# Performance work log

Hardware: AMD Instinct MI355X
Metric: run time of the kernel (lower is better)

The kernel has to match this reference:

```python
import jax, jax.numpy as jnp
import numpy as np

BS, L, H, D = 4, 1024, 12, 768   # docs, seq len, attn heads, hidden
NE, M, P = 42, 96, 42 * 42        # max entities (min_height), mentions/doc, ht pairs
OFFSET = 1                        # bert/roberta [CLS] offset


def setup_inputs() -> dict:
    key = jax.random.key(0)
    k1, k2, k3, k4, k5 = jax.random.split(key, 5)
    sequence_output = jax.random.normal(k1, (BS, L, D), jnp.float32)
    attention = jax.random.uniform(k2, (BS, H, L, L), jnp.float32)
    mention_pos = jax.random.randint(k3, (BS, M), 0, L - OFFSET - 1).astype(jnp.int32)
    mention_entity = jnp.sort(jax.random.randint(k4, (BS, M), 0, NE), axis=-1).astype(jnp.int32)
    hts = jax.random.randint(k5, (BS, P, 2), 0, NE).astype(jnp.int32)
    return {"sequence_output": sequence_output, "attention": attention,
            "mention_pos": mention_pos, "mention_entity": mention_entity, "hts": hts}


def _per_doc_entities(seq, att, pos, ent):
    # seq [L,D], att [H,L,L], pos [M] mention token idx, ent [M] entity segment id
    idx = pos + OFFSET
    m_emb = seq[idx]                              # [M,D]  gathered mention embeddings
    m_att = jnp.transpose(att[:, idx], (1, 0, 2))  # [M,H,L] gathered mention attentions
    counts = jax.ops.segment_sum(jnp.ones((M,), seq.dtype), ent, num_segments=NE)
    has = counts > 0
    # mean-pool attentions per entity (zeros for empty entities, as in torch code)
    e_att = jax.ops.segment_sum(m_att, ent, num_segments=NE) / jnp.maximum(counts, 1.0)[:, None, None]
    # stable logsumexp-pool embeddings per entity
    seg_max = jax.ops.segment_max(m_emb, ent, num_segments=NE)      # -inf for empty segments
    seg_max = jnp.where(has[:, None], seg_max, 0.0)
    seg_sum = jax.ops.segment_sum(jnp.exp(m_emb - seg_max[ent]), ent, num_segments=NE)
    e_emb = jnp.where(has[:, None], jnp.log(jnp.maximum(seg_sum, 1e-30)) + seg_max, 0.0)
    return e_emb, e_att                           # [NE,D], [NE,H,L]


def _channel_map(seq, e_att):
    # all-pairs (h_att * t_att).mean(heads), normalize over tokens, contract with seq
    pair = jnp.einsum('ahl,bhl->abl', e_att, e_att) / H      # [NE,NE,L]
    pair = pair / (pair.sum(-1, keepdims=True) + 1e-5)
    return jnp.einsum('abl,ld->abd', pair, seq)              # [NE,NE,D]


def reference(sequence_output, attention, mention_pos, mention_entity, hts):
    e_emb, e_att = jax.vmap(_per_doc_entities)(sequence_output, attention,
                                               mention_pos, mention_entity)
    hss = jax.vmap(lambda emb, ht: emb[ht[:, 0]])(e_emb, hts).reshape(BS * P, D)
    tss = jax.vmap(lambda emb, ht: emb[ht[:, 1]])(e_emb, hts).reshape(BS * P, D)
    feature_map = jax.vmap(_channel_map)(sequence_output, e_att)  # [BS,NE,NE,D]
    return hss, tss, feature_map
```

## Files before the change

### kernel.cpp

```cpp
#include <hip/hip_runtime.h>
#include <hip/hip_bf16.h>

#define BSZ   4
#define LSEQ  1024
#define NH    12
#define DDIM  768
#define NEN   42
#define NM    96
#define NPAIR (NEN*NEN)
#define OFF   1

typedef short bf16x8 __attribute__((ext_vector_type(8)));
typedef float f32x4  __attribute__((ext_vector_type(4)));

__device__ __forceinline__ float bf2f(unsigned short u) {
    union { unsigned u; float f; } c; c.u = ((unsigned)u) << 16; return c.f;
}

typedef const __attribute__((address_space(1))) unsigned int glb_u32;
typedef __attribute__((address_space(3))) unsigned int lds_u32;
__device__ __forceinline__ void glds16(const void* g, void* l) {
    __builtin_amdgcn_global_load_lds((glb_u32*)g, (lds_u32*)l, 16, 0, 0);
}

#define EMB_CNT  (BSZ*NEN*DDIM)
#define EATT_CNT (BSZ*NEN*NH*LSEQ)
#define PTIL_CNT ((size_t)BSZ*NPAIR*LSEQ)

#define PREP_EMB_BLKS  (BSZ*NEN*3)
#define PREP_ATT_BLKS  (BSZ*NEN*NH)
#define PREP_T_BLKS    ((LSEQ/32)*(DDIM/32)*BSZ)
#define PREP_TOTAL     (PREP_EMB_BLKS + PREP_ATT_BLKS + PREP_T_BLKS)

#define TEN   6
#define NTILE 7
#define NTRIT (NTILE*(NTILE+1)/2)
#define LCHK  256
#define PAIR_TOTAL (NTRIT*(LSEQ/LCHK)*BSZ)

#define BM 128
#define BN 64
#define BK 64
#define MT 14
#define NT (DDIM/BN)
#define FMAP_BLKS (MT*NT*BSZ)
#define GATH_BLKS (BSZ*NPAIR/4)
#define TAIL_TOTAL (FMAP_BLKS + GATH_BLKS)

__global__ __launch_bounds__(256) void prep_kernel(
        const float* __restrict__ seq,
        const float* __restrict__ att,
        const int* __restrict__ mpos,
        const int* __restrict__ ment,
        float* __restrict__ e_emb,
        __hip_bfloat16* __restrict__ e_att,
        __hip_bfloat16* __restrict__ seqT) {
    __shared__ __align__(16) char smraw[4352];
    const int bid = blockIdx.x;
    const int t = threadIdx.x;

    if (bid < PREP_EMB_BLKS) {
        int chunk = bid % 3;
        int e = (bid / 3) % NEN;
        int b = bid / (3 * NEN);
        int* sp   = (int*)smraw;
        int* se   = sp + NM;
        int* list = se + NM;
        int* pcnt = list + NM;
        if (t < NM) { sp[t] = mpos[b*NM + t] + OFF; se[t] = ment[b*NM + t]; }
        __syncthreads();
        if (t == 0) {
            int c = 0;
            for (int m = 0; m < NM; ++m) if (se[m] == e) list[c++] = sp[m];
            pcnt[0] = c;
        }
        __syncthreads();
        int cnt = pcnt[0];
        int d = chunk * 256 + t;
        const float* sq = seq + (size_t)b * LSEQ * DDIM + d;
        float mx = -1e30f;
        for (int m = 0; m < cnt; ++m) mx = fmaxf(mx, sq[(size_t)list[m] * DDIM]);
        float out = 0.f;
        if (cnt) {
            float s = 0.f;
            for (int m = 0; m < cnt; ++m) s += expf(sq[(size_t)list[m] * DDIM] - mx);
            out = logf(fmaxf(s, 1e-30f)) + mx;
        }
        e_emb[((size_t)b*NEN + e)*DDIM + d] = out;
    } else if (bid < PREP_EMB_BLKS + PREP_ATT_BLKS) {
        int id = bid - PREP_EMB_BLKS;
        int h = id % NH;
        int e = (id / NH) % NEN;
        int b = id / (NH * NEN);
        int* sp = (int*)smraw;
        int* se = sp + NM;
        if (t < NM) { sp[t] = mpos[b*NM + t] + OFF; se[t] = ment[b*NM + t]; }
        __syncthreads();
        const float* ab = att + ((size_t)(b*NH + h)) * LSEQ * LSEQ;
        float4 acc = {0.f, 0.f, 0.f, 0.f};
        int cnt = 0;
        for (int m = 0; m < NM; ++m) {
            if (se[m] == e) {
                ++cnt;
                float4 v = ((const float4*)(ab + (size_t)sp[m]*LSEQ))[t];
                acc.x += v.x; acc.y += v.y; acc.z += v.z; acc.w += v.w;
            }
        }
        float inv = cnt ? 1.f / (float)cnt : 0.f;
        union { ushort4 u4; __hip_bfloat16 hh[4]; } pk;
        pk.hh[0] = __float2bfloat16(acc.x * inv);
        pk.hh[1] = __float2bfloat16(acc.y * inv);
        pk.hh[2] = __float2bfloat16(acc.z * inv);
        pk.hh[3] = __float2bfloat16(acc.w * inv);
        ((ushort4*)(e_att + ((size_t)(b*NEN + e)*NH + h)*LSEQ))[t] = pk.u4;
    } else {
        int id = bid - PREP_EMB_BLKS - PREP_ATT_BLKS;
        int l0 = (id % (LSEQ/32)) * 32;
        int d0 = ((id / (LSEQ/32)) % (DDIM/32)) * 32;
        int b  = id / ((LSEQ/32) * (DDIM/32));
        float (*tile)[33] = (float(*)[33])smraw;
        int l = t >> 3, dq = (t & 7) * 4;
        float4 v = *(const float4*)(seq + ((size_t)b*LSEQ + l0 + l)*DDIM + d0 + dq);
        tile[l][dq+0] = v.x; tile[l][dq+1] = v.y;
        tile[l][dq+2] = v.z; tile[l][dq+3] = v.w;
        __syncthreads();
        int d = t >> 3, lq = (t & 7) * 4;
        union { ushort4 u4; __hip_bfloat16 h[4]; } pk;
        pk.h[0] = __float2bfloat16(tile[lq+0][d]);
        pk.h[1] = __float2bfloat16(tile[lq+1][d]);
        pk.h[2] = __float2bfloat16(tile[lq+2][d]);
        pk.h[3] = __float2bfloat16(tile[lq+3][d]);
        *(ushort4*)(seqT + ((size_t)b*DDIM + d0 + d)*LSEQ + l0 + lq) = pk.u4;
    }
}

__global__ __launch_bounds__(256) void pair_tile_kernel(
        const __hip_bfloat16* __restrict__ e_att,
        __hip_bfloat16* __restrict__ ptil) {
    const int bid = blockIdx.x;
    const int t = threadIdx.x;
    int tri = bid % NTRIT;
    int lc  = (bid / NTRIT) % (LSEQ/LCHK);
    int b   = bid / (NTRIT * (LSEQ/LCHK));
    int ta = 0, rem = tri;
    while (rem >= NTILE - ta) { rem -= NTILE - ta; ++ta; }
    int tb = ta + rem;
    int l = lc * LCHK + t;

    const __hip_bfloat16* ebase = e_att + (size_t)b*NEN*NH*LSEQ + l;
    float s[TEN][TEN];
    #pragma unroll
    for (int i = 0; i < TEN; ++i)
        #pragma unroll
        for (int j = 0; j < TEN; ++j) s[i][j] = 0.f;

    #pragma unroll 4
    for (int h = 0; h < NH; ++h) {
        float xa[TEN], xb[TEN];
        #pragma unroll
        for (int e = 0; e < TEN; ++e)
            xa[e] = bf2f(*(const unsigned short*)(ebase + ((size_t)(ta*TEN+e)*NH + h)*LSEQ));
        #pragma unroll
        for (int e = 0; e < TEN; ++e)
            xb[e] = bf2f(*(const unsigned short*)(ebase + ((size_t)(tb*TEN+e)*NH + h)*LSEQ));
        #pragma unroll
        for (int i = 0; i < TEN; ++i)
            #pragma unroll
            for (int j = 0; j < TEN; ++j)
                s[i][j] += xa[i] * xb[j];
    }

    __hip_bfloat16* pbase = ptil + (size_t)b*NPAIR*LSEQ + l;
    #pragma unroll
    for (int i = 0; i < TEN; ++i) {
        #pragma unroll
        for (int j = 0; j < TEN; ++j) {
            union { unsigned short u; __hip_bfloat16 h; } pk;
            pk.h = __float2bfloat16(s[i][j]);
            int pa = ta*TEN + i, pb = tb*TEN + j;
            *(unsigned short*)(pbase + (size_t)(pa*NEN + pb)*LSEQ) = pk.u;
            if (ta != tb)
                *(unsigned short*)(pbase + (size_t)(pb*NEN + pa)*LSEQ) = pk.u;
        }
    }
}

__global__ __launch_bounds__(256) void tail_kernel(
        const __hip_bfloat16* __restrict__ ptil,
        const __hip_bfloat16* __restrict__ seqT,
        const float* __restrict__ e_emb,
        const int* __restrict__ hts,
        float* __restrict__ out_h,
        float* __restrict__ out_t,
        float* __restrict__ fmap) {
    __shared__ __hip_bfloat16 As[2][BM*BK];
    __shared__ __hip_bfloat16 Bs[2][BN*BK];
    const int bid = blockIdx.x;
    const int t = threadIdx.x;

    if (bid >= FMAP_BLKS) {
        int id4  = bid - FMAP_BLKS;
        int grp  = t >> 6;
        int lane = t & 63;
        int id   = id4 * 4 + grp;
        int b    = id / NPAIR;
        int hi = hts[id*2 + 0];
        int ti = hts[id*2 + 1];
        const float4* eh = (const float4*)(e_emb + ((size_t)(b*NEN + hi))*DDIM);
        const float4* et = (const float4*)(e_emb + ((size_t)(b*NEN + ti))*DDIM);
        float4* oh = (float4*)(out_h + (size_t)id*DDIM);
        float4* ot = (float4*)(out_t + (size_t)id*DDIM);
        #pragma unroll
        for (int i = 0; i < 3; ++i) {
            oh[lane + 64*i] = eh[lane + 64*i];
            ot[lane + 64*i] = et[lane + 64*i];
        }
        return;
    }

    const int lane = t & 63;
    const int wid  = t >> 6;
    const int wr   = wid >> 1;
    const int wc   = wid & 1;
    const int bx = bid % MT, by = (bid / MT) % NT, b = bid / (MT*NT);
    const int r0 = bx * BM, c0 = by * BN;

    const char* Ab  = (const char*)(ptil + (size_t)b * NPAIR * LSEQ);
    const char* Btb = (const char*)(seqT + (size_t)b * DDIM * LSEQ);
    char* AsB = (char*)As;
    char* BsB = (char*)Bs;

    const f32x4 zero = {0.f, 0.f, 0.f, 0.f};
    f32x4 acc[4][2];
    #pragma unroll
    for (int m = 0; m < 4; ++m)
        #pragma unroll
        for (int n = 0; n < 2; ++n) acc[m][n] = zero;

    const int fr = lane & 15, kg = lane >> 4;
    const int rs_r = t >> 1, rs_h = t & 1;
    float rsum = 0.f;

#define STAGE(buf, k0)                                                        \
    {                                                                         \
        _Pragma("unroll")                                                     \
        for (int i = 0; i < 4; ++i) {                                         \
            int L = wid*4096 + i*1024 + lane*16;                              \
            int r = L >> 7, beta = L & 127;                                   \
            glds16(Ab + (size_t)(r0 + r)*(LSEQ*2) + (k0)*2                    \
                      + (beta ^ ((r & 7) << 4)), AsB + (buf)*16384 + L);      \
        }                                                                     \
        _Pragma("unroll")                                                     \
        for (int i = 0; i < 2; ++i) {                                         \
            int L = wid*2048 + i*1024 + lane*16;                              \
            int c = L >> 7, beta = L & 127;                                   \
            glds16(Btb + (size_t)(c0 + c)*(LSEQ*2) + (k0)*2                   \
                      + (beta ^ ((c & 7) << 4)), BsB + (buf)*8192 + L);       \
        }                                                                     \
    }

    STAGE(0, 0);
    __syncthreads();

    int cur = 0;
    for (int ki = 0; ki < LSEQ/BK; ++ki) {
        if (ki + 1 < LSEQ/BK) STAGE(cur ^ 1, (ki + 1) * BK);

        const __hip_bfloat16* Ac = (const __hip_bfloat16*)(AsB + cur*16384);
        const __hip_bfloat16* Bc = (const __hip_bfloat16*)(BsB + cur*8192);

        #pragma unroll
        for (int jj = 0; jj < 4; ++jj) {
            int e0 = (rs_h*32 + jj*8) ^ ((rs_r & 7) << 3);
            bf16x8 v = *(const bf16x8*)(Ac + rs_r*64 + e0);
            #pragma unroll
            for (int j = 0; j < 8; ++j) rsum += bf2f((unsigned short)v[j]);
        }

        #pragma unroll
        for (int ks = 0; ks < 2; ++ks) {
            bf16x8 af[4], bfv[2];
            #pragma unroll
            for (int m = 0; m < 4; ++m) {
                int R = wr*64 + m*16 + fr;
                int e0 = (ks*32 + kg*8) ^ ((R & 7) << 3);
                af[m] = *(const bf16x8*)(Ac + R*64 + e0);
            }
            #pragma unroll
            for (int n = 0; n < 2; ++n) {
                int C = wc*32 + n*16 + fr;
                int e0 = (ks*32 + kg*8) ^ ((C & 7) << 3);
                bfv[n] = *(const bf16x8*)(Bc + C*64 + e0);
            }
            #pragma unroll
            for (int m = 0; m < 4; ++m)
                #pragma unroll
                for (int n = 0; n < 2; ++n)
                    acc[m][n] = __builtin_amdgcn_mfma_f32_16x16x32_bf16(
                                    af[m], bfv[n], acc[m][n], 0, 0, 0);
        }
        __syncthreads();
        cur ^= 1;
    }

    float rtot = rsum + __shfl_down(rsum, 1);
    float* ssum = (float*)AsB;
    if ((t & 1) == 0) ssum[rs_r] = rtot;
    __syncthreads();

    #pragma unroll
    for (int m = 0; m < 4; ++m) {
        int lr0 = wr*64 + m*16 + kg*4;
        #pragma unroll
        for (int i = 0; i < 4; ++i) {
            int lr = lr0 + i;
            int row = r0 + lr;
            if (row < NPAIR) {
                float sc = 1.f / (ssum[lr] + (float)NH * 1e-5f);
                #pragma unroll
                for (int n = 0; n < 2; ++n) {
                    int col = c0 + wc*32 + n*16 + fr;
                    fmap[((size_t)b*NPAIR + row)*DDIM + col] = acc[m][n][i] * sc;
                }
            }
        }
    }
#undef STAGE
}

extern "C" void kernel_launch(void* const* d_in, const int* in_sizes, int n_in,
                              void* d_out, int out_size, void* d_ws, size_t ws_size,
                              hipStream_t stream) {
    const float* seq  = (const float*)d_in[0];
    const float* att  = (const float*)d_in[1];
    const int*   mpos = (const int*)d_in[2];
    const int*   ment = (const int*)d_in[3];
    const int*   hts  = (const int*)d_in[4];

    float* ws_f  = (float*)d_ws;
    float* e_emb = ws_f;
    __hip_bfloat16* e_att = (__hip_bfloat16*)(ws_f + EMB_CNT);
    __hip_bfloat16* ptil  = e_att + EATT_CNT;
    __hip_bfloat16* seqT  = ptil + PTIL_CNT;

    float* out_h = (float*)d_out;
    float* out_t = out_h + (size_t)BSZ*NPAIR*DDIM;
    float* fmap  = out_t + (size_t)BSZ*NPAIR*DDIM;

    hipLaunchKernelGGL(prep_kernel, dim3(PREP_TOTAL), dim3(256), 0, stream,
                       seq, att, mpos, ment, e_emb, e_att, seqT);
    hipLaunchKernelGGL(pair_tile_kernel, dim3(PAIR_TOTAL), dim3(256), 0, stream,
                       e_att, ptil);
    hipLaunchKernelGGL(tail_kernel, dim3(TAIL_TOTAL), dim3(256), 0, stream,
                       ptil, seqT, e_emb, hts, out_h, out_t, fmap);
}
```

Before: 59.73 us.

## Rebalance kernel stages and compute pair row sums in pair-tile kernel

Splits the entity attention pooling into its own kernel and moves the seq transpose and embedding pooling into the pair-tile kernel, so independent work overlaps with pair-product computation. The pair-tile blocks now reduce per-row sums over their L chunk in fp32 and write partial sums to a workspace. The GEMM tail reads those partials instead of summing the A tile from LDS each K step. Tail block indices are also remapped across groups of eight. This removes per-iteration ALU and LDS work from the GEMM loop. It adds a shuffle reduction and extra small global writes in the pair stage.

Result: faster. 56.17 us (-6.0%).

```diff
diff --git a/kernel.cpp b/kernel.cpp
--- a/kernel.cpp
+++ b/kernel.cpp
@@ -23,20 +23,22 @@
     __builtin_amdgcn_global_load_lds((glb_u32*)g, (lds_u32*)l, 16, 0, 0);
 }
 
+#define NLC   4
 #define EMB_CNT  (BSZ*NEN*DDIM)
+#define PSUM_CNT (BSZ*NLC*NPAIR)
 #define EATT_CNT (BSZ*NEN*NH*LSEQ)
 #define PTIL_CNT ((size_t)BSZ*NPAIR*LSEQ)
 
-#define PREP_EMB_BLKS  (BSZ*NEN*3)
-#define PREP_ATT_BLKS  (BSZ*NEN*NH)
-#define PREP_T_BLKS    ((LSEQ/32)*(DDIM/32)*BSZ)
-#define PREP_TOTAL     (PREP_EMB_BLKS + PREP_ATT_BLKS + PREP_T_BLKS)
+#define ATT_TOTAL (BSZ*NEN*NH)
 
 #define TEN   6
 #define NTILE 7
 #define NTRIT (NTILE*(NTILE+1)/2)
 #define LCHK  256
-#define PAIR_TOTAL (NTRIT*(LSEQ/LCHK)*BSZ)
+#define PAIR_BLKS (NTRIT*NLC*BSZ)
+#define T_BLKS    ((LSEQ/32)*(DDIM/32)*BSZ)
+#define EMB_BLKS  (BSZ*NEN*3)
+#define MID2_TOTAL (PAIR_BLKS + T_BLKS + EMB_BLKS)
 
 #define BM 128
 #define BN 64
@@ -47,22 +49,148 @@
 #define GATH_BLKS (BSZ*NPAIR/4)
 #define TAIL_TOTAL (FMAP_BLKS + GATH_BLKS)
 
-__global__ __launch_bounds__(256) void prep_kernel(
-        const float* __restrict__ seq,
+__global__ __launch_bounds__(256) void att_kernel(
         const float* __restrict__ att,
         const int* __restrict__ mpos,
         const int* __restrict__ ment,
-        float* __restrict__ e_emb,
-        __hip_bfloat16* __restrict__ e_att,
-        __hip_bfloat16* __restrict__ seqT) {
+        __hip_bfloat16* __restrict__ e_att) {
+    __shared__ int sp[NM];
+    __shared__ int se[NM];
+    int id = blockIdx.x;
+    int h = id % NH;
+    int e = (id / NH) % NEN;
+    int b = id / (NH * NEN);
+    int t = threadIdx.x;
+    if (t < NM) { sp[t] = mpos[b*NM + t] + OFF; se[t] = ment[b*NM + t]; }
+    __syncthreads();
+    const float* ab = att + ((size_t)(b*NH + h)) * LSEQ * LSEQ;
+    float4 acc = {0.f, 0.f, 0.f, 0.f};
+    int cnt = 0;
+    for (int m = 0; m < NM; ++m) {
+        if (se[m] == e) {
+            ++cnt;
+            float4 v = ((const float4*)(ab + (size_t)sp[m]*LSEQ))[t];
+            acc.x += v.x; acc.y += v.y; acc.z += v.z; acc.w += v.w;
+        }
+    }
+    float inv = cnt ? 1.f / (float)cnt : 0.f;
+    union { ushort4 u4; __hip_bfloat16 hh[4]; } pk;
+    pk.hh[0] = __float2bfloat16(acc.x * inv);
+    pk.hh[1] = __float2bfloat16(acc.y * inv);
+    pk.hh[2] = __float2bfloat16(acc.z * inv);
+    pk.hh[3] = __float2bfloat16(acc.w * inv);
+    ((ushort4*)(e_att + ((size_t)(b*NEN + e)*NH + h)*LSEQ))[t] = pk.u4;
+}
+
+__global__ __launch_bounds__(256) void mid2_kernel(
+        const float* __restrict__ seq,
+        const __hip_bfloat16* __restrict__ e_att,
+        const int* __restrict__ mpos,
+        const int* __restrict__ ment,
+        __hip_bfloat16* __restrict__ ptil,
+        float* __restrict__ psum,
+        __hip_bfloat16* __restrict__ seqT,
+        float* __restrict__ e_emb) {
     __shared__ __align__(16) char smraw[4352];
     const int bid = blockIdx.x;
     const int t = threadIdx.x;
 
-    if (bid < PREP_EMB_BLKS) {
-        int chunk = bid % 3;
-        int e = (bid / 3) % NEN;
-        int b = bid / (3 * NEN);
+    if (bid < PAIR_BLKS) {
+        int tri = bid % NTRIT;
+        int lc  = (bid / NTRIT) % NLC;
+        int b   = bid / (NTRIT * NLC);
+        int ta = 0, rem = tri;
+        while (rem >= NTILE - ta) { rem -= NTILE - ta; ++ta; }
+        int tb = ta + rem;
+        int l = lc * LCHK + t;
+
+        const __hip_bfloat16* ebase = e_att + (size_t)b*NEN*NH*LSEQ + l;
+        float s[TEN][TEN];
+        #pragma unroll
+        for (int i = 0; i < TEN; ++i)
+            #pragma unroll
+            for (int j = 0; j < TEN; ++j) s[i][j] = 0.f;
+
+        #pragma unroll 4
+        for (int h = 0; h < NH; ++h) {
+            float xa[TEN], xb[TEN];
+            #pragma unroll
+            for (int e = 0; e < TEN; ++e)
+                xa[e] = bf2f(*(const unsigned short*)(ebase + ((size_t)(ta*TEN+e)*NH + h)*LSEQ));
+            #pragma unroll
+            for (int e = 0; e < TEN; ++e)
+                xb[e] = bf2f(*(const unsigned short*)(ebase + ((size_t)(tb*TEN+e)*NH + h)*LSEQ));
+            #pragma unroll
+            for (int i = 0; i < TEN; ++i)
+                #pragma unroll
+                for (int j = 0; j < TEN; ++j)
+                    s[i][j] += xa[i] * xb[j];
+        }
+
+        __hip_bfloat16* pbase = ptil + (size_t)b*NPAIR*LSEQ + l;
+        #pragma unroll
+        for (int i = 0; i < TEN; ++i) {
+            #pragma unroll
+            for (int j = 0; j < TEN; ++j) {
+                union { unsigned short u; __hip_bfloat16 h; } pk;
+                pk.h = __float2bfloat16(s[i][j]);
+                int pa = ta*TEN + i, pb = tb*TEN + j;
+                *(unsigned short*)(pbase + (size_t)(pa*NEN + pb)*LSEQ) = pk.u;
+                if (ta != tb)
+                    *(unsigned short*)(pbase + (size_t)(pb*NEN + pa)*LSEQ) = pk.u;
+            }
+        }
+
+        int lane = t & 63, w = t >> 6;
+        float (*redp)[TEN*TEN] = (float(*)[TEN*TEN])smraw;
+        float keep = 0.f;
+        #pragma unroll
+        for (int i = 0; i < TEN; ++i) {
+            #pragma unroll
+            for (int j = 0; j < TEN; ++j) {
+                float v = s[i][j];
+                v += __shfl_xor(v,  1, 64);
+                v += __shfl_xor(v,  2, 64);
+                v += __shfl_xor(v,  4, 64);
+                v += __shfl_xor(v,  8, 64);
+                v += __shfl_xor(v, 16, 64);
+                v += __shfl_xor(v, 32, 64);
+                if (lane == i*TEN + j) keep = v;
+            }
+        }
+        if (lane < TEN*TEN) redp[w][lane] = keep;
+        __syncthreads();
+        if (t < TEN*TEN) {
+            float v = redp[0][t] + redp[1][t] + redp[2][t] + redp[3][t];
+            int i = t / TEN, j = t % TEN;
+            int pa = ta*TEN + i, pb = tb*TEN + j;
+            float* ps = psum + ((size_t)(b*NLC + lc))*NPAIR;
+            ps[pa*NEN + pb] = v;
+            if (ta != tb) ps[pb*NEN + pa] = v;
+        }
+    } else if (bid < PAIR_BLKS + T_BLKS) {
+        int id = bid - PAIR_BLKS;
+        int l0 = (id % (LSEQ/32)) * 32;
+        int d0 = ((id / (LSEQ/32)) % (DDIM/32)) * 32;
+        int b  = id / ((LSEQ/32) * (DDIM/32));
+        float (*tile)[33] = (float(*)[33])smraw;
+        int l = t >> 3, dq = (t & 7) * 4;
+        float4 v = *(const float4*)(seq + ((size_t)b*LSEQ + l0 + l)*DDIM + d0 + dq);
+        tile[l][dq+0] = v.x; tile[l][dq+1] = v.y;
+        tile[l][dq+2] = v.z; tile[l][dq+3] = v.w;
+        __syncthreads();
+        int d = t >> 3, lq = (t & 7) * 4;
+        union { ushort4 u4; __hip_bfloat16 h[4]; } pk;
+        pk.h[0] = __float2bfloat16(tile[lq+0][d]);
+        pk.h[1] = __float2bfloat16(tile[lq+1][d]);
+        pk.h[2] = __float2bfloat16(tile[lq+2][d]);
+        pk.h[3] = __float2bfloat16(tile[lq+3][d]);
+        *(ushort4*)(seqT + ((size_t)b*DDIM + d0 + d)*LSEQ + l0 + lq) = pk.u4;
+    } else {
+        int id = bid - PAIR_BLKS - T_BLKS;
+        int chunk = id % 3;
+        int e = (id / 3) % NEN;
+        int b = id / (3 * NEN);
         int* sp   = (int*)smraw;
         int* se   = sp + NM;
         int* list = se + NM;
@@ -87,107 +215,13 @@
             out = logf(fmaxf(s, 1e-30f)) + mx;
         }
         e_emb[((size_t)b*NEN + e)*DDIM + d] = out;
-    } else if (bid < PREP_EMB_BLKS + PREP_ATT_BLKS) {
-        int id = bid - PREP_EMB_BLKS;
-        int h = id % NH;
-        int e = (id / NH) % NEN;
-        int b = id / (NH * NEN);
-        int* sp = (int*)smraw;
-        int* se = sp + NM;
-        if (t < NM) { sp[t] = mpos[b*NM + t] + OFF; se[t] = ment[b*NM + t]; }
-        __syncthreads();
-        const float* ab = att + ((size_t)(b*NH + h)) * LSEQ * LSEQ;
-        float4 acc = {0.f, 0.f, 0.f, 0.f};
-        int cnt = 0;
-        for (int m = 0; m < NM; ++m) {
-            if (se[m] == e) {
-                ++cnt;
-                float4 v = ((const float4*)(ab + (size_t)sp[m]*LSEQ))[t];
-                acc.x += v.x; acc.y += v.y; acc.z += v.z; acc.w += v.w;
-            }
-        }
-        float inv = cnt ? 1.f / (float)cnt : 0.f;
-        union { ushort4 u4; __hip_bfloat16 hh[4]; } pk;
-        pk.hh[0] = __float2bfloat16(acc.x * inv);
-        pk.hh[1] = __float2bfloat16(acc.y * inv);
-        pk.hh[2] = __float2bfloat16(acc.z * inv);
-        pk.hh[3] = __float2bfloat16(acc.w * inv);
-        ((ushort4*)(e_att + ((size_t)(b*NEN + e)*NH + h)*LSEQ))[t] = pk.u4;
-    } else {
-        int id = bid - PREP_EMB_BLKS - PREP_ATT_BLKS;
-        int l0 = (id % (LSEQ/32)) * 32;
-        int d0 = ((id / (LSEQ/32)) % (DDIM/32)) * 32;
-        int b  = id / ((LSEQ/32) * (DDIM/32));
-        float (*tile)[33] = (float(*)[33])smraw;
-        int l = t >> 3, dq = (t & 7) * 4;
-        float4 v = *(const float4*)(seq + ((size_t)b*LSEQ + l0 + l)*DDIM + d0 + dq);
-        tile[l][dq+0] = v.x; tile[l][dq+1] = v.y;
-        tile[l][dq+2] = v.z; tile[l][dq+3] = v.w;
-        __syncthreads();
-        int d = t >> 3, lq = (t & 7) * 4;
-        union { ushort4 u4; __hip_bfloat16 h[4]; } pk;
-        pk.h[0] = __float2bfloat16(tile[lq+0][d]);
-        pk.h[1] = __float2bfloat16(tile[lq+1][d]);
-        pk.h[2] = __float2bfloat16(tile[lq+2][d]);
-        pk.h[3] = __float2bfloat16(tile[lq+3][d]);
-        *(ushort4*)(seqT + ((size_t)b*DDIM + d0 + d)*LSEQ + l0 + lq) = pk.u4;
-    }
-}
-
-__global__ __launch_bounds__(256) void pair_tile_kernel(
-        const __hip_bfloat16* __restrict__ e_att,
-        __hip_bfloat16* __restrict__ ptil) {
-    const int bid = blockIdx.x;
-    const int t = threadIdx.x;
-    int tri = bid % NTRIT;
-    int lc  = (bid / NTRIT) % (LSEQ/LCHK);
-    int b   = bid / (NTRIT * (LSEQ/LCHK));
-    int ta = 0, rem = tri;
-    while (rem >= NTILE - ta) { rem -= NTILE - ta; ++ta; }
-    int tb = ta + rem;
-    int l = lc * LCHK + t;
-
-    const __hip_bfloat16* ebase = e_att + (size_t)b*NEN*NH*LSEQ + l;
-    float s[TEN][TEN];
-    #pragma unroll
-    for (int i = 0; i < TEN; ++i)
-        #pragma unroll
-        for (int j = 0; j < TEN; ++j) s[i][j] = 0.f;
-
-    #pragma unroll 4
-    for (int h = 0; h < NH; ++h) {
-        float xa[TEN], xb[TEN];
-        #pragma unroll
-        for (int e = 0; e < TEN; ++e)
-            xa[e] = bf2f(*(const unsigned short*)(ebase + ((size_t)(ta*TEN+e)*NH + h)*LSEQ));
-        #pragma unroll
-        for (int e = 0; e < TEN; ++e)
-            xb[e] = bf2f(*(const unsigned short*)(ebase + ((size_t)(tb*TEN+e)*NH + h)*LSEQ));
-        #pragma unroll
-        for (int i = 0; i < TEN; ++i)
-            #pragma unroll
-            for (int j = 0; j < TEN; ++j)
-                s[i][j] += xa[i] * xb[j];
-    }
-
-    __hip_bfloat16* pbase = ptil + (size_t)b*NPAIR*LSEQ + l;
-    #pragma unroll
-    for (int i = 0; i < TEN; ++i) {
-        #pragma unroll
-        for (int j = 0; j < TEN; ++j) {
-            union { unsigned short u; __hip_bfloat16 h; } pk;
-            pk.h = __float2bfloat16(s[i][j]);
-            int pa = ta*TEN + i, pb = tb*TEN + j;
-            *(unsigned short*)(pbase + (size_t)(pa*NEN + pb)*LSEQ) = pk.u;
-            if (ta != tb)
-                *(unsigned short*)(pbase + (size_t)(pb*NEN + pa)*LSEQ) = pk.u;
-        }
     }
 }
 
 __global__ __launch_bounds__(256) void tail_kernel(
         const __hip_bfloat16* __restrict__ ptil,
         const __hip_bfloat16* __restrict__ seqT,
+        const float* __restrict__ psum,
         const float* __restrict__ e_emb,
         const int* __restrict__ hts,
         float* __restrict__ out_h,
@@ -218,11 +252,12 @@
         return;
     }
 
+    int tile = (bid & 7) * (FMAP_BLKS/8) + (bid >> 3);
     const int lane = t & 63;
     const int wid  = t >> 6;
     const int wr   = wid >> 1;
     const int wc   = wid & 1;
-    const int bx = bid % MT, by = (bid / MT) % NT, b = bid / (MT*NT);
+    const int bx = tile % MT, by = (tile / MT) % NT, b = tile / (MT*NT);
     const int r0 = bx * BM, c0 = by * BN;
 
     const char* Ab  = (const char*)(ptil + (size_t)b * NPAIR * LSEQ);
@@ -238,8 +273,6 @@
         for (int n = 0; n < 2; ++n) acc[m][n] = zero;
 
     const int fr = lane & 15, kg = lane >> 4;
-    const int rs_r = t >> 1, rs_h = t & 1;
-    float rsum = 0.f;
 
 #define STAGE(buf, k0)                                                        \
     {                                                                         \
@@ -270,14 +303,6 @@
         const __hip_bfloat16* Bc = (const __hip_bfloat16*)(BsB + cur*8192);
 
         #pragma unroll
-        for (int jj = 0; jj < 4; ++jj) {
-            int e0 = (rs_h*32 + jj*8) ^ ((rs_r & 7) << 3);
-            bf16x8 v = *(const bf16x8*)(Ac + rs_r*64 + e0);
-            #pragma unroll
-            for (int j = 0; j < 8; ++j) rsum += bf2f((unsigned short)v[j]);
-        }
-
-        #pragma unroll
         for (int ks = 0; ks < 2; ++ks) {
             bf16x8 af[4], bfv[2];
             #pragma unroll
@@ -303,20 +328,17 @@
         cur ^= 1;
     }
 
-    float rtot = rsum + __shfl_down(rsum, 1);
-    float* ssum = (float*)AsB;
-    if ((t & 1) == 0) ssum[rs_r] = rtot;
-    __syncthreads();
-
+    const float* psb = psum + (size_t)b * NLC * NPAIR;
     #pragma unroll
     for (int m = 0; m < 4; ++m) {
         int lr0 = wr*64 + m*16 + kg*4;
         #pragma unroll
         for (int i = 0; i < 4; ++i) {
-            int lr = lr0 + i;
-            int row = r0 + lr;
+            int row = r0 + lr0 + i;
             if (row < NPAIR) {
-                float sc = 1.f / (ssum[lr] + (float)NH * 1e-5f);
+                float S = psb[row] + psb[NPAIR + row]
+                        + psb[2*NPAIR + row] + psb[3*NPAIR + row];
+                float sc = 1.f / (S + (float)NH * 1e-5f);
                 #pragma unroll
                 for (int n = 0; n < 2; ++n) {
                     int col = c0 + wc*32 + n*16 + fr;
@@ -339,7 +361,8 @@
 
     float* ws_f  = (float*)d_ws;
     float* e_emb = ws_f;
-    __hip_bfloat16* e_att = (__hip_bfloat16*)(ws_f + EMB_CNT);
+    float* psum  = ws_f + EMB_CNT;
+    __hip_bfloat16* e_att = (__hip_bfloat16*)(ws_f + EMB_CNT + PSUM_CNT);
     __hip_bfloat16* ptil  = e_att + EATT_CNT;
     __hip_bfloat16* seqT  = ptil + PTIL_CNT;
 
@@ -347,10 +370,10 @@
     float* out_t = out_h + (size_t)BSZ*NPAIR*DDIM;
     float* fmap  = out_t + (size_t)BSZ*NPAIR*DDIM;
 
-    hipLaunchKernelGGL(prep_kernel, dim3(PREP_TOTAL), dim3(256), 0, stream,
-                       seq, att, mpos, ment, e_emb, e_att, seqT);
-    hipLaunchKernelGGL(pair_tile_kernel, dim3(PAIR_TOTAL), dim3(256), 0, stream,
-                       e_att, ptil);
+    hipLaunchKernelGGL(att_kernel, dim3(ATT_TOTAL), dim3(256), 0, stream,
+                       att, mpos, ment, e_att);
+    hipLaunchKernelGGL(mid2_kernel, dim3(MID2_TOTAL), dim3(256), 0, stream,
+                       seq, e_att, mpos, ment, ptil, psum, seqT, e_emb);
     hipLaunchKernelGGL(tail_kernel, dim3(TAIL_TOTAL), dim3(256), 0, stream,
-                       ptil, seqT, e_emb, hts, out_h, out_t, fmap);
-}
+                       ptil, seqT, psum, e_emb, hts, out_h, out_t, fmap);
+}
```
